# Kernel tuning notes

Hardware: AMD Instinct MI355X
Metric: run time of the kernel (lower is better)

## Reference

```python
import jax, jax.numpy as jnp
import numpy as np

N_NODES = 100000
N_EDGES = 1600000
HEADS = 4
HID = 64
IN_CH = 3
N_GRAPHS = 64
NEG_SLOPE = 0.2  # PyG GATConv default


def _gat_layer(x, src, dst, W, a_src, a_dst, b):
    """PyG GATConv with concat=False (head-mean), eval mode (no dropout)."""
    N = x.shape[0]
    xl = (x @ W).reshape(N, HEADS, HID)            # [N,H,C]
    es = (xl * a_src).sum(-1)                       # [N,H] alpha_src
    ed = (xl * a_dst).sum(-1)                       # [N,H] alpha_dst
    e = jax.nn.leaky_relu(es[src] + ed[dst], NEG_SLOPE)  # [E,H]
    # segment softmax over incoming edges of each dst node
    m = jax.ops.segment_max(e, dst, num_segments=N)      # [N,H]
    ex = jnp.exp(e - m[dst])
    s = jax.ops.segment_sum(ex, dst, num_segments=N)     # [N,H]
    alpha = ex / s[dst]                                   # [E,H]
    msg = xl[src] * alpha[:, :, None]                     # [E,H,C]
    out = jax.ops.segment_sum(msg, dst, num_segments=N)   # [N,H,C]
    return out.mean(axis=1) + b                            # head mean + bias


def setup_inputs() -> dict:
    key = jax.random.key(0)
    ks = jax.random.split(key, 12)
    x = jax.random.normal(ks[0], (N_NODES, IN_CH), dtype=jnp.float32)
    edge_index = jax.random.randint(ks[1], (2, N_EDGES), 0, N_NODES, dtype=jnp.int64)
    batch_ids = jnp.sort(jax.random.randint(ks[2], (N_NODES,), 0, N_GRAPHS, dtype=jnp.int64))
    def glorot(k, shape, fan_in):
        return jax.random.normal(k, shape, dtype=jnp.float32) / np.sqrt(fan_in)
    W1 = glorot(ks[3], (IN_CH, HEADS * HID), IN_CH)
    a_src1 = glorot(ks[4], (HEADS, HID), HID)
    a_dst1 = glorot(ks[5], (HEADS, HID), HID)
    b1 = jnp.zeros((HID,), dtype=jnp.float32)
    W2 = glorot(ks[6], (HID, HEADS * HID), HID)
    a_src2 = glorot(ks[7], (HEADS, HID), HID)
    a_dst2 = glorot(ks[8], (HEADS, HID), HID)
    b2 = jnp.zeros((HID,), dtype=jnp.float32)
    return {"x": x, "edge_index": edge_index, "batch_ids": batch_ids,
            "W1": W1, "a_src1": a_src1, "a_dst1": a_dst1, "b1": b1,
            "W2": W2, "a_src2": a_src2, "a_dst2": a_dst2, "b2": b2}


def reference(x, edge_index, batch_ids, W1, a_src1, a_dst1, b1, W2, a_src2, a_dst2, b2):
    src, dst = edge_index[0], edge_index[1]
    h = jax.nn.relu(_gat_layer(x, src, dst, W1, a_src1, a_dst1, b1))
    h = jax.nn.relu(_gat_layer(h, src, dst, W2, a_src2, a_dst2, b2))
    # global_add_pool
    g = jax.ops.segment_sum(h, batch_ids, num_segments=N_GRAPHS)  # [G, HID]
    return g
```

## Files before the change

kernel.cpp:

```cpp
#include <hip/hip_runtime.h>
#include <math.h>

#define HEADS 4
#define HID 64
#define BSHIFT 7
#define BWIDTH 128
#define CCAP 4096
#define DCHUNK 8192

typedef __attribute__((ext_vector_type(8))) short short8;
typedef __attribute__((ext_vector_type(4))) float f32x4;

__device__ __forceinline__ float lrelu(float x) { return x > 0.f ? x : 0.2f * x; }

__device__ __forceinline__ unsigned short bf16r(float f) {
    unsigned u = __float_as_uint(f);
    unsigned r = (u + 0x7FFFu + ((u >> 16) & 1u)) >> 16;
    return (unsigned short)r;
}
__device__ __forceinline__ float bf2f(unsigned short u) {
    return __uint_as_float(((unsigned)u) << 16);
}

__device__ __forceinline__ float wred_sum(float v) {
#pragma unroll
    for (int o = 32; o > 0; o >>= 1) v += __shfl_xor(v, o);
    return v;
}
__device__ __forceinline__ float red16_sum(float v) {
#pragma unroll
    for (int o = 8; o > 0; o >>= 1) v += __shfl_xor(v, o);
    return v;
}

__global__ void k_binit(int* __restrict__ bcnt, int NBUCK) {
    int i = threadIdx.x;
    if (i < NBUCK) bcnt[i] = 0;
}

__global__ void k_bhist(const int* __restrict__ dstI, int* __restrict__ bcnt,
                        int E, int NBUCK) {
    __shared__ int h[1024];
    for (int i = threadIdx.x; i < NBUCK; i += 256) h[i] = 0;
    __syncthreads();
    int stride = gridDim.x * 256;
    for (int e = blockIdx.x * 256 + threadIdx.x; e < E; e += stride)
        atomicAdd(&h[dstI[e] >> BSHIFT], 1);
    __syncthreads();
    for (int i = threadIdx.x; i < NBUCK; i += 256)
        if (h[i]) atomicAdd(&bcnt[i], h[i]);
}

__global__ void k_bscan(const int* __restrict__ bcnt, int* __restrict__ bbase,
                        int* __restrict__ gcur, int* __restrict__ off,
                        int NBUCK, int N, int E) {
    __shared__ int lds[1024];
    int t = threadIdx.x;
    int v = (t < NBUCK) ? bcnt[t] : 0;
    lds[t] = v;
    __syncthreads();
    for (int s = 1; s < 1024; s <<= 1) {
        int u = (t >= s) ? lds[t - s] : 0;
        __syncthreads();
        lds[t] += u;
        __syncthreads();
    }
    if (t < NBUCK) {
        int b = lds[t] - v;
        bbase[t] = b;
        gcur[t] = b;
    }
    if (t == 0) { bbase[NBUCK] = E; off[N] = E; }
}

__global__ void k_bdist(const int* __restrict__ srcI, const int* __restrict__ dstI,
                        int* __restrict__ gcur, unsigned* __restrict__ pairs,
                        int E, int NBUCK) {
    __shared__ int h[1024];
    __shared__ int cur[1024];
    for (int i = threadIdx.x; i < NBUCK; i += 1024) h[i] = 0;
    __syncthreads();
    int base = blockIdx.x * DCHUNK;
    int sr[8], dr[8];
#pragma unroll
    for (int k = 0; k < 8; k++) {
        int e = base + threadIdx.x + k * 1024;
        if (e < E) {
            sr[k] = srcI[e];
            dr[k] = dstI[e];
            atomicAdd(&h[dr[k] >> BSHIFT], 1);
        } else dr[k] = -1;
    }
    __syncthreads();
    for (int i = threadIdx.x; i < NBUCK; i += 1024)
        cur[i] = h[i] ? atomicAdd(&gcur[i], h[i]) : 0;
    __syncthreads();
#pragma unroll
    for (int k = 0; k < 8; k++) {
        if (dr[k] >= 0) {
            int b = dr[k] >> BSHIFT;
            int p = atomicAdd(&cur[b], 1);
            pairs[p] = ((unsigned)sr[k] << BSHIFT) | ((unsigned)dr[k] & (BWIDTH - 1));
        }
    }
}

__global__ void k_bcsr(const unsigned* __restrict__ pairs, const int* __restrict__ bbase,
                       int* __restrict__ off, int* __restrict__ csr, int N) {
    __shared__ int cnt[BWIDTH];
    __shared__ int scan[BWIDTH];
    __shared__ int cur[BWIDTH];
    __shared__ int stage[CCAP];
    int b = blockIdx.x;
    int nodeBase = b << BSHIFT;
    int nNodes = N - nodeBase;
    if (nNodes > BWIDTH) nNodes = BWIDTH;
    int e0 = bbase[b], e1 = bbase[b + 1];
    int ecnt = e1 - e0;
    if (threadIdx.x < BWIDTH) cnt[threadIdx.x] = 0;
    __syncthreads();
    for (int i = threadIdx.x; i < ecnt; i += 256)
        atomicAdd(&cnt[pairs[e0 + i] & (BWIDTH - 1)], 1);
    __syncthreads();
    if (threadIdx.x < BWIDTH)
        scan[threadIdx.x] = (threadIdx.x < nNodes) ? cnt[threadIdx.x] : 0;
    __syncthreads();
    for (int s = 1; s < BWIDTH; s <<= 1) {
        int u = 0;
        if (threadIdx.x < BWIDTH && threadIdx.x >= s) u = scan[threadIdx.x - s];
        __syncthreads();
        if (threadIdx.x < BWIDTH) scan[threadIdx.x] += u;
        __syncthreads();
    }
    if (threadIdx.x < nNodes) {
        int ex = scan[threadIdx.x] - cnt[threadIdx.x];
        off[nodeBase + threadIdx.x] = e0 + ex;
        cur[threadIdx.x] = ex;
    }
    __syncthreads();
    for (int i = threadIdx.x; i < ecnt; i += 256) {
        unsigned pr = pairs[e0 + i];
        int l = atomicAdd(&cur[pr & (BWIDTH - 1)], 1);
        int src = (int)(pr >> BSHIFT);
        if (l < CCAP) stage[l] = src;
        else csr[e0 + l] = src;
    }
    __syncthreads();
    int lim = ecnt < CCAP ? ecnt : CCAP;
    for (int i = threadIdx.x; i < lim; i += 256) csr[e0 + i] = stage[i];
}

__global__ void k_prep(const float* __restrict__ W, const float* __restrict__ asrc,
                       const float* __restrict__ adst, float* __restrict__ p_src,
                       float* __restrict__ p_dst, int K) {
    int wid = (blockIdx.x * blockDim.x + threadIdx.x) >> 6;
    int lane = threadIdx.x & 63;
    int total = K * 4 * 2;
    if (wid >= total) return;
    int which = wid / (K * 4);
    int hk = wid % (K * 4);
    int h = hk / K, k = hk % K;
    const float* a = which ? adst : asrc;
    float v = W[(size_t)k * 256 + h * 64 + lane] * a[h * 64 + lane];
    v = wred_sum(v);
    if (lane == 0) (which ? p_dst : p_src)[h * K + k] = v;
}

__global__ void k_w2bt(const float* __restrict__ W2, unsigned short* __restrict__ W2bt,
                       float* __restrict__ out, int outTotal) {
    int i = blockIdx.x * 256 + threadIdx.x;
    int c = i >> 8, kh = i & 255;
    int h = kh >> 6, kf = kh & 63;
    W2bt[i] = bf16r(W2[kf * 256 + h * 64 + c]);
    if (i < outTotal) out[i] = 0.f;
}

__global__ void k_esed1(const float* __restrict__ x, const float* __restrict__ ps,
                        const float* __restrict__ pd, float* __restrict__ es,
                        float* __restrict__ ed, int N) {
    int n = blockIdx.x * blockDim.x + threadIdx.x;
    if (n >= N) return;
    float x0 = x[n * 3], x1 = x[n * 3 + 1], x2 = x[n * 3 + 2];
    float4 s, d;
    s.x = x0 * ps[0] + x1 * ps[1] + x2 * ps[2];
    s.y = x0 * ps[3] + x1 * ps[4] + x2 * ps[5];
    s.z = x0 * ps[6] + x1 * ps[7] + x2 * ps[8];
    s.w = x0 * ps[9] + x1 * ps[10] + x2 * ps[11];
    d.x = x0 * pd[0] + x1 * pd[1] + x2 * pd[2];
    d.y = x0 * pd[3] + x1 * pd[4] + x2 * pd[5];
    d.z = x0 * pd[6] + x1 * pd[7] + x2 * pd[8];
    d.w = x0 * pd[9] + x1 * pd[10] + x2 * pd[11];
    ((float4*)es)[n] = s;
    ((float4*)ed)[n] = d;
}

__global__ void k_agg1(const int* __restrict__ off, const int* __restrict__ csr,
                       const float* __restrict__ es, const float* __restrict__ ed,
                       const float* __restrict__ x, const float* __restrict__ W1,
                       const float* __restrict__ b1, const float* __restrict__ qs,
                       const float* __restrict__ qd, unsigned short* __restrict__ houtb,
                       float* __restrict__ es2, float* __restrict__ ed2, int N) {
    int grp = (blockIdx.x * blockDim.x + threadIdx.x) >> 4;
    int l = threadIdx.x & 15;
    int wid = grp;
    bool active = wid < N;
    int o0 = 0, deg = 0;
    float4 edv = make_float4(0.f, 0.f, 0.f, 0.f);
    if (active) {
        o0 = off[wid];
        deg = off[wid + 1] - o0;
        edv = ((const float4*)ed)[wid];
    }

    float t0 = 0.f, t1 = 0.f, t2 = 0.f, t3 = 0.f;
    float a00 = 0, a01 = 0, a02 = 0, a10 = 0, a11 = 0, a12 = 0;
    float a20 = 0, a21 = 0, a22 = 0, a30 = 0, a31 = 0, a32 = 0;
    for (int j = l; j < deg; j += 16) {
        int s = csr[o0 + j];
        float4 ev = ((const float4*)es)[s];
        float e0 = __expf(lrelu(ev.x + edv.x));
        float e1 = __expf(lrelu(ev.y + edv.y));
        float e2 = __expf(lrelu(ev.z + edv.z));
        float e3 = __expf(lrelu(ev.w + edv.w));
        float xv0 = x[s * 3], xv1 = x[s * 3 + 1], xv2 = x[s * 3 + 2];
        t0 += e0; t1 += e1; t2 += e2; t3 += e3;
        a00 += e0 * xv0; a01 += e0 * xv1; a02 += e0 * xv2;
        a10 += e1 * xv0; a11 += e1 * xv1; a12 += e1 * xv2;
        a20 += e2 * xv0; a21 += e2 * xv1; a22 += e2 * xv2;
        a30 += e3 * xv0; a31 += e3 * xv1; a32 += e3 * xv2;
    }
    t0 = red16_sum(t0); t1 = red16_sum(t1); t2 = red16_sum(t2); t3 = red16_sum(t3);
    float i0 = t0 > 0.f ? 1.f / t0 : 0.f;
    float i1 = t1 > 0.f ? 1.f / t1 : 0.f;
    float i2 = t2 > 0.f ? 1.f / t2 : 0.f;
    float i3 = t3 > 0.f ? 1.f / t3 : 0.f;
    a00 = red16_sum(a00) * i0; a01 = red16_sum(a01) * i0; a02 = red16_sum(a02) * i0;
    a10 = red16_sum(a10) * i1; a11 = red16_sum(a11) * i1; a12 = red16_sum(a12) * i1;
    a20 = red16_sum(a20) * i2; a21 = red16_sum(a21) * i2; a22 = red16_sum(a22) * i2;
    a30 = red16_sum(a30) * i3; a31 = red16_sum(a31) * i3; a32 = red16_sum(a32) * i3;

    if (!active) return;

    const float4* W1f = (const float4*)W1;
    float4 r = make_float4(0.f, 0.f, 0.f, 0.f);
    float ah[4][3] = {{a00, a01, a02}, {a10, a11, a12}, {a20, a21, a22}, {a30, a31, a32}};
#pragma unroll
    for (int k = 0; k < 3; k++) {
#pragma unroll
        for (int h = 0; h < 4; h++) {
            float4 wv = W1f[k * 64 + h * 16 + l];
            float a = ah[h][k];
            r.x += a * wv.x; r.y += a * wv.y; r.z += a * wv.z; r.w += a * wv.w;
        }
    }
    float4 bv = ((const float4*)b1)[l];
    float4 hv;
    hv.x = fmaxf(0.25f * r.x + bv.x, 0.f);
    hv.y = fmaxf(0.25f * r.y + bv.y, 0.f);
    hv.z = fmaxf(0.25f * r.z + bv.z, 0.f);
    hv.w = fmaxf(0.25f * r.w + bv.w, 0.f);
    ((ushort4*)houtb)[(size_t)wid * 16 + l] =
        make_ushort4(bf16r(hv.x), bf16r(hv.y), bf16r(hv.z), bf16r(hv.w));

    const float4* qsf = (const float4*)qs;
    const float4* qdf = (const float4*)qd;
    float ps[4], pd[4];
#pragma unroll
    for (int h = 0; h < 4; h++) {
        float4 q = qsf[h * 16 + l];
        ps[h] = red16_sum(hv.x * q.x + hv.y * q.y + hv.z * q.z + hv.w * q.w);
        float4 p = qdf[h * 16 + l];
        pd[h] = red16_sum(hv.x * p.x + hv.y * p.y + hv.z * p.z + hv.w * p.w);
    }
    if (l == 0) {
        ((float4*)es2)[wid] = make_float4(ps[0], ps[1], ps[2], ps[3]);
        ((float4*)ed2)[wid] = make_float4(pd[0], pd[1], pd[2], pd[3]);
    }
}

#define NS 16
__global__ void k_agg2(const int* __restrict__ off, const int* __restrict__ csr,
                       const float* __restrict__ es, const float* __restrict__ ed,
                       const unsigned short* __restrict__ houtb,
                       unsigned short* __restrict__ aggb, int N) {
    __shared__ float exl[NS * 64 * 4];
    __shared__ int   sl[NS * 64];
    __shared__ float minv[NS * 4];
    __shared__ int   meta[NS * 2];

    for (int i = threadIdx.x; i < NS * 64; i += 256) {
        ((float4*)exl)[i] = make_float4(0.f, 0.f, 0.f, 0.f);
        sl[i] = 0;
    }
    __syncthreads();

    int l = threadIdx.x & 15;
    int slot = threadIdx.x >> 4;
    int wid = blockIdx.x * NS + slot;
    bool active = wid < N;
    int o0 = 0, deg = 0;
    float4 edv = make_float4(0.f, 0.f, 0.f, 0.f);
    if (active) {
        o0 = off[wid];
        deg = off[wid + 1] - o0;
        edv = ((const float4*)ed)[wid];
    }

    float t0 = 0.f, t1 = 0.f, t2 = 0.f, t3 = 0.f;
    for (int j = l; j < deg; j += 16) {
        int s = csr[o0 + j];
        float4 ev = ((const float4*)es)[s];
        float e0 = __expf(lrelu(ev.x + edv.x));
        float e1 = __expf(lrelu(ev.y + edv.y));
        float e2 = __expf(lrelu(ev.z + edv.z));
        float e3 = __expf(lrelu(ev.w + edv.w));
        if (j < 64) {
            ((float4*)exl)[slot * 64 + j] = make_float4(e0, e1, e2, e3);
            sl[slot * 64 + j] = s;
        }
        t0 += e0; t1 += e1; t2 += e2; t3 += e3;
    }
    t0 = red16_sum(t0); t1 = red16_sum(t1); t2 = red16_sum(t2); t3 = red16_sum(t3);
    if (l == 0) {
        minv[slot * 4 + 0] = t0 > 0.f ? 1.f / t0 : 0.f;
        minv[slot * 4 + 1] = t1 > 0.f ? 1.f / t1 : 0.f;
        minv[slot * 4 + 2] = t2 > 0.f ? 1.f / t2 : 0.f;
        minv[slot * 4 + 3] = t3 > 0.f ? 1.f / t3 : 0.f;
        meta[slot * 2 + 0] = o0;
        meta[slot * 2 + 1] = deg;
    }
    __syncthreads();

    int lane = threadIdx.x & 63;
    int w = threadIdx.x >> 6;
    int half = lane >> 5;
    int c2 = lane & 31;
    for (int sidx = 0; sidx < 4; sidx++) {
        int slot2 = w * 4 + sidx;
        int nd = blockIdx.x * NS + slot2;
        if (nd >= N) continue;
        int o0b = meta[slot2 * 2 + 0], degb = meta[slot2 * 2 + 1];
        float iv0 = minv[slot2 * 4 + 0], iv1 = minv[slot2 * 4 + 1];
        float iv2 = minv[slot2 * 4 + 2], iv3 = minv[slot2 * 4 + 3];

        float p00 = 0.f, p01 = 0.f, p10 = 0.f, p11 = 0.f;
        float p20 = 0.f, p21 = 0.f, p30 = 0.f, p31 = 0.f;
        const float4* EX = ((const float4*)exl) + slot2 * 64;
        const int* S = sl + slot2 * 64;
        int dmain = degb < 64 ? degb : 64;
        int d8 = (dmain + 7) & ~7;
        for (int j = 0; j < d8; j += 8) {
            float4 a0 = EX[j + half];
            float4 a1 = EX[j + 2 + half];
            float4 a2 = EX[j + 4 + half];
            float4 a3 = EX[j + 6 + half];
            int s0 = S[j + half], s1 = S[j + 2 + half];
            int s2 = S[j + 4 + half], s3 = S[j + 6 + half];
            unsigned u0 = *(const unsigned*)(houtb + (size_t)s0 * 64 + 2 * c2);
            unsigned u1 = *(const unsigned*)(houtb + (size_t)s1 * 64 + 2 * c2);
            unsigned u2 = *(const unsigned*)(houtb + (size_t)s2 * 64 + 2 * c2);
            unsigned u3 = *(const unsigned*)(houtb + (size_t)s3 * 64 + 2 * c2);
            float v0l = __uint_as_float(u0 << 16), v0h = __uint_as_float(u0 & 0xffff0000u);
            float v1l = __uint_as_float(u1 << 16), v1h = __uint_as_float(u1 & 0xffff0000u);
            float v2l = __uint_as_float(u2 << 16), v2h = __uint_as_float(u2 & 0xffff0000u);
            float v3l = __uint_as_float(u3 << 16), v3h = __uint_as_float(u3 & 0xffff0000u);
            p00 += a0.x * v0l + a1.x * v1l + a2.x * v2l + a3.x * v3l;
            p01 += a0.x * v0h + a1.x * v1h + a2.x * v2h + a3.x * v3h;
            p10 += a0.y * v0l + a1.y * v1l + a2.y * v2l + a3.y * v3l;
            p11 += a0.y * v0h + a1.y * v1h + a2.y * v2h + a3.y * v3h;
            p20 += a0.z * v0l + a1.z * v1l + a2.z * v2l + a3.z * v3l;
            p21 += a0.z * v0h + a1.z * v1h + a2.z * v2h + a3.z * v3h;
            p30 += a0.w * v0l + a1.w * v1l + a2.w * v2l + a3.w * v3l;
            p31 += a0.w * v0h + a1.w * v1h + a2.w * v2h + a3.w * v3h;
        }
        if (degb > 64) {
            float4 edv2 = ((const float4*)ed)[nd];
            for (int j = 64 + half; j < degb; j += 2) {
                int s = csr[o0b + j];
                float4 ev = ((const float4*)es)[s];
                float e0 = __expf(lrelu(ev.x + edv2.x));
                float e1 = __expf(lrelu(ev.y + edv2.y));
                float e2 = __expf(lrelu(ev.z + edv2.z));
                float e3 = __expf(lrelu(ev.w + edv2.w));
                unsigned u = *(const unsigned*)(houtb + (size_t)s * 64 + 2 * c2);
                float vl = __uint_as_float(u << 16), vh = __uint_as_float(u & 0xffff0000u);
                p00 += e0 * vl; p01 += e0 * vh;
                p10 += e1 * vl; p11 += e1 * vh;
                p20 += e2 * vl; p21 += e2 * vh;
                p30 += e3 * vl; p31 += e3 * vh;
            }
        }
        p00 += __shfl_xor(p00, 32); p01 += __shfl_xor(p01, 32);
        p10 += __shfl_xor(p10, 32); p11 += __shfl_xor(p11, 32);
        p20 += __shfl_xor(p20, 32); p21 += __shfl_xor(p21, 32);
        p30 += __shfl_xor(p30, 32); p31 += __shfl_xor(p31, 32);

        if (half == 0) {
            size_t b = (size_t)nd * 256;
            unsigned w0 = (unsigned)bf16r(p00 * iv0) | ((unsigned)bf16r(p01 * iv0) << 16);
            unsigned w1 = (unsigned)bf16r(p10 * iv1) | ((unsigned)bf16r(p11 * iv1) << 16);
            unsigned w2 = (unsigned)bf16r(p20 * iv2) | ((unsigned)bf16r(p21 * iv2) << 16);
            unsigned w3 = (unsigned)bf16r(p30 * iv3) | ((unsigned)bf16r(p31 * iv3) << 16);
            *(unsigned*)(aggb + b + 2 * c2)        = w0;
            *(unsigned*)(aggb + b + 64 + 2 * c2)   = w1;
            *(unsigned*)(aggb + b + 128 + 2 * c2)  = w2;
            *(unsigned*)(aggb + b + 192 + 2 * c2)  = w3;
        }
    }
}

__global__ void k_out2(const unsigned short* __restrict__ aggb,
                       const unsigned short* __restrict__ W2bt,
                       const float* __restrict__ b2, const int* __restrict__ batch,
                       float* __restrict__ out, int N) {
    int w = threadIdx.x >> 6, lane = threadIdx.x & 63;
    int nodeBase = blockIdx.x * 64 + w * 16;
    int m = lane & 15;
    int quad = lane >> 4;
    const short* A = (const short*)aggb + (size_t)(nodeBase + m) * 256 + quad * 8;
    const short* B = (const short*)W2bt;

    f32x4 acc0 = {0.f, 0.f, 0.f, 0.f}, acc1 = {0.f, 0.f, 0.f, 0.f};
    f32x4 acc2 = {0.f, 0.f, 0.f, 0.f}, acc3 = {0.f, 0.f, 0.f, 0.f};
#pragma unroll
    for (int kk = 0; kk < 8; kk++) {
        short8 af = *(const short8*)(A + kk * 32);
        short8 b0 = *(const short8*)(B + (size_t)(0 * 16 + m) * 256 + kk * 32 + quad * 8);
        short8 b1v = *(const short8*)(B + (size_t)(1 * 16 + m) * 256 + kk * 32 + quad * 8);
        short8 b2v = *(const short8*)(B + (size_t)(2 * 16 + m) * 256 + kk * 32 + quad * 8);
        short8 b3v = *(const short8*)(B + (size_t)(3 * 16 + m) * 256 + kk * 32 + quad * 8);
        acc0 = __builtin_amdgcn_mfma_f32_16x16x32_bf16(af, b0, acc0, 0, 0, 0);
        acc1 = __builtin_amdgcn_mfma_f32_16x16x32_bf16(af, b1v, acc1, 0, 0, 0);
        acc2 = __builtin_amdgcn_mfma_f32_16x16x32_bf16(af, b2v, acc2, 0, 0, 0);
        acc3 = __builtin_amdgcn_mfma_f32_16x16x32_bf16(af, b3v, acc3, 0, 0, 0);
    }
    f32x4 accs[4] = {acc0, acc1, acc2, acc3};

    float vals[4][4];
#pragma unroll
    for (int cb = 0; cb < 4; cb++) {
        float bv = b2[cb * 16 + m];
#pragma unroll
        for (int r = 0; r < 4; r++)
            vals[cb][r] = fmaxf(0.25f * accs[cb][r] + bv, 0.f);
    }

    bool fast = (nodeBase + 15 < N);
    int g0 = 0;
    if (fast) {
        g0 = batch[nodeBase];
        int g1 = batch[nodeBase + 15];
        fast = (g0 == g1);
    }
    if (fast) {
#pragma unroll
        for (int cb = 0; cb < 4; cb++) {
            float s = vals[cb][0] + vals[cb][1] + vals[cb][2] + vals[cb][3];
            s += __shfl_xor(s, 16);
            s += __shfl_xor(s, 32);
            if (quad == 0) atomicAdd(&out[g0 * 64 + cb * 16 + m], s);
        }
    } else {
#pragma unroll
        for (int r = 0; r < 4; r++) {
            int node = nodeBase + quad * 4 + r;
            if (node < N) {
                int g = batch[node];
#pragma unroll
                for (int cb = 0; cb < 4; cb++)
                    atomicAdd(&out[g * 64 + cb * 16 + m], vals[cb][r]);
            }
        }
    }
}

extern "C" void kernel_launch(void* const* d_in, const int* in_sizes, int n_in,
                              void* d_out, int out_size, void* d_ws, size_t ws_size,
                              hipStream_t stream) {
    const float* x   = (const float*)d_in[0];
    const int*   ei  = (const int*)d_in[1];
    const int*   bat = (const int*)d_in[2];
    const float* W1  = (const float*)d_in[3];
    const float* as1 = (const float*)d_in[4];
    const float* ad1 = (const float*)d_in[5];
    const float* b1  = (const float*)d_in[6];
    const float* W2  = (const float*)d_in[7];
    const float* as2 = (const float*)d_in[8];
    const float* ad2 = (const float*)d_in[9];
    const float* b2  = (const float*)d_in[10];
    float* out = (float*)d_out;

    int N = in_sizes[0] / 3;
    int E = in_sizes[1] / 2;
    int G = out_size / 64;
    const int* srcI = ei;
    const int* dstI = ei + E;
    int NBUCK = (N + BWIDTH - 1) >> BSHIFT;

    float* fw = (float*)d_ws;
    size_t fo = 0;
    unsigned short* aggb = (unsigned short*)fw; fo += (size_t)N * 128;
    unsigned short* houtb = (unsigned short*)(fw + fo); fo += (size_t)N * 32;
    float* esA   = fw + fo; fo += (size_t)N * 4;
    float* edA   = fw + fo; fo += (size_t)N * 4;
    float* esB   = fw + fo; fo += (size_t)N * 4;
    float* edB   = fw + fo; fo += (size_t)N * 4;
    float* p1s   = fw + fo; fo += 64;
    float* p1d   = fw + fo; fo += 64;
    float* qs    = fw + fo; fo += 256;
    float* qd    = fw + fo; fo += 256;
    unsigned short* W2bt = (unsigned short*)(fw + fo); fo += 64 * 256 / 2;
    int* iw = (int*)(fw + fo);
    size_t io = 0;
    unsigned* pairs = (unsigned*)iw; io += E;
    int* csr    = iw + io; io += E;
    int* off    = iw + io; io += N + 1;
    int* bbase  = iw + io; io += 1025;
    int* gcur   = iw + io; io += 1024;
    int* bcnt   = iw + io; io += 1024;

    int nThrBlk = (N + 255) / 256;
    int nGrpBlk = (N + 15) / 16;

    k_binit<<<1, 1024, 0, stream>>>(bcnt, NBUCK);
    k_bhist<<<256, 256, 0, stream>>>(dstI, bcnt, E, NBUCK);
    k_bscan<<<1, 1024, 0, stream>>>(bcnt, bbase, gcur, off, NBUCK, N, E);
    k_bdist<<<(E + DCHUNK - 1) / DCHUNK, 1024, 0, stream>>>(srcI, dstI, gcur, pairs, E, NBUCK);
    k_bcsr<<<NBUCK, 256, 0, stream>>>(pairs, bbase, off, csr, N);

    k_prep<<<(3 * 8 * 64 + 255) / 256, 256, 0, stream>>>(W1, as1, ad1, p1s, p1d, 3);
    k_prep<<<(64 * 8 * 64 + 255) / 256, 256, 0, stream>>>(W2, as2, ad2, qs, qd, 64);
    k_w2bt<<<64, 256, 0, stream>>>(W2, W2bt, out, G * 64);

    k_esed1<<<nThrBlk, 256, 0, stream>>>(x, p1s, p1d, esA, edA, N);
    k_agg1<<<nGrpBlk, 256, 0, stream>>>(off, csr, esA, edA, x, W1, b1, qs, qd,
                                        houtb, esB, edB, N);

    k_agg2<<<nGrpBlk, 256, 0, stream>>>(off, csr, esB, edB, houtb, aggb, N);
    k_out2<<<(N + 63) / 64, 256, 0, stream>>>(aggb, W2bt, b2, bat, out, N);
}
```

Baseline: 254.2 us.

## Merge weight-prep kernels, drop LDS zero-init, vectorize bf16 aggregation FMAs

```diff
diff --git a/kernel.cpp b/kernel.cpp
--- a/kernel.cpp
+++ b/kernel.cpp
@@ -10,6 +10,7 @@
 
 typedef __attribute__((ext_vector_type(8))) short short8;
 typedef __attribute__((ext_vector_type(4))) float f32x4;
+typedef __attribute__((ext_vector_type(2))) float f32x2;
 
 __device__ __forceinline__ float lrelu(float x) { return x > 0.f ? x : 0.2f * x; }
 
@@ -18,8 +19,11 @@
     unsigned r = (u + 0x7FFFu + ((u >> 16) & 1u)) >> 16;
     return (unsigned short)r;
 }
-__device__ __forceinline__ float bf2f(unsigned short u) {
-    return __uint_as_float(((unsigned)u) << 16);
+__device__ __forceinline__ f32x2 unpk(unsigned u) {
+    f32x2 r;
+    r.x = __uint_as_float(u << 16);
+    r.y = __uint_as_float(u & 0xffff0000u);
+    return r;
 }
 
 __device__ __forceinline__ float wred_sum(float v) {
@@ -150,10 +154,12 @@
     for (int i = threadIdx.x; i < lim; i += 256) csr[e0 + i] = stage[i];
 }
 
-__global__ void k_prep(const float* __restrict__ W, const float* __restrict__ asrc,
-                       const float* __restrict__ adst, float* __restrict__ p_src,
-                       float* __restrict__ p_dst, int K) {
-    int wid = (blockIdx.x * blockDim.x + threadIdx.x) >> 6;
+__device__ __forceinline__ void prep_body(const float* __restrict__ W,
+                                          const float* __restrict__ asrc,
+                                          const float* __restrict__ adst,
+                                          float* __restrict__ p_src,
+                                          float* __restrict__ p_dst, int K, int blk) {
+    int wid = blk * 4 + (threadIdx.x >> 6);
     int lane = threadIdx.x & 63;
     int total = K * 4 * 2;
     if (wid >= total) return;
@@ -166,13 +172,25 @@
     if (lane == 0) (which ? p_dst : p_src)[h * K + k] = v;
 }
 
-__global__ void k_w2bt(const float* __restrict__ W2, unsigned short* __restrict__ W2bt,
-                       float* __restrict__ out, int outTotal) {
-    int i = blockIdx.x * 256 + threadIdx.x;
-    int c = i >> 8, kh = i & 255;
-    int h = kh >> 6, kf = kh & 63;
-    W2bt[i] = bf16r(W2[kf * 256 + h * 64 + c]);
-    if (i < outTotal) out[i] = 0.f;
+__global__ void k_prep_all(const float* __restrict__ W1, const float* __restrict__ as1,
+                           const float* __restrict__ ad1, const float* __restrict__ W2,
+                           const float* __restrict__ as2, const float* __restrict__ ad2,
+                           float* __restrict__ p1s, float* __restrict__ p1d,
+                           float* __restrict__ qs, float* __restrict__ qd,
+                           unsigned short* __restrict__ W2bt, float* __restrict__ out,
+                           int outTotal) {
+    int b = blockIdx.x;
+    if (b < 6) {
+        prep_body(W1, as1, ad1, p1s, p1d, 3, b);
+    } else if (b < 134) {
+        prep_body(W2, as2, ad2, qs, qd, 64, b - 6);
+    } else {
+        int i = (b - 134) * 256 + threadIdx.x;
+        int c = i >> 8, kh = i & 255;
+        int h = kh >> 6, kf = kh & 63;
+        W2bt[i] = bf16r(W2[kf * 256 + h * 64 + c]);
+        if (i < outTotal) out[i] = 0.f;
+    }
 }
 
 __global__ void k_esed1(const float* __restrict__ x, const float* __restrict__ ps,
@@ -288,12 +306,6 @@
     __shared__ float minv[NS * 4];
     __shared__ int   meta[NS * 2];
 
-    for (int i = threadIdx.x; i < NS * 64; i += 256) {
-        ((float4*)exl)[i] = make_float4(0.f, 0.f, 0.f, 0.f);
-        sl[i] = 0;
-    }
-    __syncthreads();
-
     int l = threadIdx.x & 15;
     int slot = threadIdx.x >> 4;
     int wid = blockIdx.x * NS + slot;
@@ -320,6 +332,14 @@
         }
         t0 += e0; t1 += e1; t2 += e2; t3 += e3;
     }
+    {
+        int dmain = deg < 64 ? deg : 64;
+        int d8 = (dmain + 7) & ~7;
+        if (dmain + l < d8) {
+            ((float4*)exl)[slot * 64 + dmain + l] = make_float4(0.f, 0.f, 0.f, 0.f);
+            sl[slot * 64 + dmain + l] = 0;
+        }
+    }
     t0 = red16_sum(t0); t1 = red16_sum(t1); t2 = red16_sum(t2); t3 = red16_sum(t3);
     if (l == 0) {
         minv[slot * 4 + 0] = t0 > 0.f ? 1.f / t0 : 0.f;
@@ -343,8 +363,7 @@
         float iv0 = minv[slot2 * 4 + 0], iv1 = minv[slot2 * 4 + 1];
         float iv2 = minv[slot2 * 4 + 2], iv3 = minv[slot2 * 4 + 3];
 
-        float p00 = 0.f, p01 = 0.f, p10 = 0.f, p11 = 0.f;
-        float p20 = 0.f, p21 = 0.f, p30 = 0.f, p31 = 0.f;
+        f32x2 q0 = {0.f, 0.f}, q1 = {0.f, 0.f}, q2 = {0.f, 0.f}, q3 = {0.f, 0.f};
         const float4* EX = ((const float4*)exl) + slot2 * 64;
         const int* S = sl + slot2 * 64;
         int dmain = degb < 64 ? degb : 64;
@@ -360,18 +379,11 @@
             unsigned u1 = *(const unsigned*)(houtb + (size_t)s1 * 64 + 2 * c2);
             unsigned u2 = *(const unsigned*)(houtb + (size_t)s2 * 64 + 2 * c2);
             unsigned u3 = *(const unsigned*)(houtb + (size_t)s3 * 64 + 2 * c2);
-            float v0l = __uint_as_float(u0 << 16), v0h = __uint_as_float(u0 & 0xffff0000u);
-            float v1l = __uint_as_float(u1 << 16), v1h = __uint_as_float(u1 & 0xffff0000u);
-            float v2l = __uint_as_float(u2 << 16), v2h = __uint_as_float(u2 & 0xffff0000u);
-            float v3l = __uint_as_float(u3 << 16), v3h = __uint_as_float(u3 & 0xffff0000u);
-            p00 += a0.x * v0l + a1.x * v1l + a2.x * v2l + a3.x * v3l;
-            p01 += a0.x * v0h + a1.x * v1h + a2.x * v2h + a3.x * v3h;
-            p10 += a0.y * v0l + a1.y * v1l + a2.y * v2l + a3.y * v3l;
-            p11 += a0.y * v0h + a1.y * v1h + a2.y * v2h + a3.y * v3h;
-            p20 += a0.z * v0l + a1.z * v1l + a2.z * v2l + a3.z * v3l;
-            p21 += a0.z * v0h + a1.z * v1h + a2.z * v2h + a3.z * v3h;
-            p30 += a0.w * v0l + a1.w * v1l + a2.w * v2l + a3.w * v3l;
-            p31 += a0.w * v0h + a1.w * v1h + a2.w * v2h + a3.w * v3h;
+            f32x2 v0 = unpk(u0), v1 = unpk(u1), v2 = unpk(u2), v3 = unpk(u3);
+            q0 += a0.x * v0; q0 += a1.x * v1; q0 += a2.x * v2; q0 += a3.x * v3;
+            q1 += a0.y * v0; q1 += a1.y * v1; q1 += a2.y * v2; q1 += a3.y * v3;
+            q2 += a0.z * v0; q2 += a1.z * v1; q2 += a2.z * v2; q2 += a3.z * v3;
+            q3 += a0.w * v0; q3 += a1.w * v1; q3 += a2.w * v2; q3 += a3.w * v3;
         }
         if (degb > 64) {
             float4 edv2 = ((const float4*)ed)[nd];
@@ -383,24 +395,21 @@
                 float e2 = __expf(lrelu(ev.z + edv2.z));
                 float e3 = __expf(lrelu(ev.w + edv2.w));
                 unsigned u = *(const unsigned*)(houtb + (size_t)s * 64 + 2 * c2);
-                float vl = __uint_as_float(u << 16), vh = __uint_as_float(u & 0xffff0000u);
-                p00 += e0 * vl; p01 += e0 * vh;
-                p10 += e1 * vl; p11 += e1 * vh;
-                p20 += e2 * vl; p21 += e2 * vh;
-                p30 += e3 * vl; p31 += e3 * vh;
+                f32x2 v = unpk(u);
+                q0 += e0 * v; q1 += e1 * v; q2 += e2 * v; q3 += e3 * v;
             }
         }
-        p00 += __shfl_xor(p00, 32); p01 += __shfl_xor(p01, 32);
-        p10 += __shfl_xor(p10, 32); p11 += __shfl_xor(p11, 32);
-        p20 += __shfl_xor(p20, 32); p21 += __shfl_xor(p21, 32);
-        p30 += __shfl_xor(p30, 32); p31 += __shfl_xor(p31, 32);
+        q0.x += __shfl_xor(q0.x, 32); q0.y += __shfl_xor(q0.y, 32);
+        q1.x += __shfl_xor(q1.x, 32); q1.y += __shfl_xor(q1.y, 32);
+        q2.x += __shfl_xor(q2.x, 32); q2.y += __shfl_xor(q2.y, 32);
+        q3.x += __shfl_xor(q3.x, 32); q3.y += __shfl_xor(q3.y, 32);
 
         if (half == 0) {
             size_t b = (size_t)nd * 256;
-            unsigned w0 = (unsigned)bf16r(p00 * iv0) | ((unsigned)bf16r(p01 * iv0) << 16);
-            unsigned w1 = (unsigned)bf16r(p10 * iv1) | ((unsigned)bf16r(p11 * iv1) << 16);
-            unsigned w2 = (unsigned)bf16r(p20 * iv2) | ((unsigned)bf16r(p21 * iv2) << 16);
-            unsigned w3 = (unsigned)bf16r(p30 * iv3) | ((unsigned)bf16r(p31 * iv3) << 16);
+            unsigned w0 = (unsigned)bf16r(q0.x * iv0) | ((unsigned)bf16r(q0.y * iv0) << 16);
+            unsigned w1 = (unsigned)bf16r(q1.x * iv1) | ((unsigned)bf16r(q1.y * iv1) << 16);
+            unsigned w2 = (unsigned)bf16r(q2.x * iv2) | ((unsigned)bf16r(q2.y * iv2) << 16);
+            unsigned w3 = (unsigned)bf16r(q3.x * iv3) | ((unsigned)bf16r(q3.y * iv3) << 16);
             *(unsigned*)(aggb + b + 2 * c2)        = w0;
             *(unsigned*)(aggb + b + 64 + 2 * c2)   = w1;
             *(unsigned*)(aggb + b + 128 + 2 * c2)  = w2;
@@ -528,9 +537,8 @@
     k_bdist<<<(E + DCHUNK - 1) / DCHUNK, 1024, 0, stream>>>(srcI, dstI, gcur, pairs, E, NBUCK);
     k_bcsr<<<NBUCK, 256, 0, stream>>>(pairs, bbase, off, csr, N);
 
-    k_prep<<<(3 * 8 * 64 + 255) / 256, 256, 0, stream>>>(W1, as1, ad1, p1s, p1d, 3);
-    k_prep<<<(64 * 8 * 64 + 255) / 256, 256, 0, stream>>>(W2, as2, ad2, qs, qd, 64);
-    k_w2bt<<<64, 256, 0, stream>>>(W2, W2bt, out, G * 64);
+    k_prep_all<<<198, 256, 0, stream>>>(W1, as1, ad1, W2, as2, ad2,
+                                        p1s, p1d, qs, qd, W2bt, out, G * 64);
 
     k_esed1<<<nThrBlk, 256, 0, stream>>>(x, p1s, p1d, esA, edA, N);
     k_agg1<<<nGrpBlk, 256, 0, stream>>>(off, csr, esA, edA, x, W1, b1, qs, qd,
```

After: 247.6 us. 1.03x faster.
